# Kernel optimization log

Measured on AMD Instinct MI355X. Metric: run time of the kernel, lower is better.

## Reference

```python
import jax, jax.numpy as jnp
import numpy as np

ARITY = 4
DEPTH = 8          # leaves = ARITY**DEPTH = 65536; internal nodes = (4**8-1)//3 = 21845
IN_DIM = 64
MEM = 128
HID = 128


def setup_inputs() -> dict:
    key = jax.random.key(0)
    ks = jax.random.split(key, 20)
    n_leaves = ARITY ** DEPTH
    n_internal = (ARITY ** DEPTH - 1) // (ARITY - 1)
    s = 0.05
    inp = {
        "inputs": jax.random.normal(ks[0], (n_leaves, IN_DIM), jnp.float32),
        "ops": jax.random.randint(ks[1], (n_internal,), 0, 2, jnp.int32),
        # MLP (all bias-free); torch Linear weight layout [out, in]
        "W1": jax.random.normal(ks[2], (MEM, IN_DIM), jnp.float32) * s,
        "W2": jax.random.normal(ks[3], (3 * MEM, MEM), jnp.float32) * s,
        "W3": jax.random.normal(ks[4], (2 * MEM, 3 * MEM), jnp.float32) * s,
        "Wp": jax.random.normal(ks[5], (MEM, 2 * MEM), jnp.float32) * s,
        # ChildSumTreeRNN
        "Wand": jax.random.normal(ks[6], (MEM, MEM), jnp.float32) * s,
        "Wor": jax.random.normal(ks[7], (MEM, MEM), jnp.float32) * s,
        "Rw1": jax.random.normal(ks[8], (HID, MEM), jnp.float32) * s,
        "Rb1": jnp.zeros((HID,), jnp.float32),
        "Rw2": jax.random.normal(ks[9], (HID, HID), jnp.float32) * s,
        "Rb2": jnp.zeros((HID,), jnp.float32),
        "Rw3": jax.random.normal(ks[10], (HID, HID), jnp.float32) * s,
        "Rb3": jnp.zeros((HID,), jnp.float32),
        "Rwp": jax.random.normal(ks[11], (1, HID), jnp.float32) * s,
        "Rbp": jnp.zeros((1,), jnp.float32),
    }
    return inp


def reference(inputs, ops, W1, W2, W3, Wp, Wand, Wor,
              Rw1, Rb1, Rw2, Rb2, Rw3, Rb3, Rwp, Rbp):
    # MLP embedding of all leaves  [n_leaves, MEM]
    h = jnp.tanh(inputs @ W1.T)
    h = jnp.tanh(h @ W2.T)
    h = jnp.tanh(h @ W3.T)
    h = jnp.tanh(h @ Wp.T)

    # ChildSumTreeRNN, level by level (children before parents).
    # Complete arity-4 tree: level l has 4**l internal nodes; ops is
    # level-ordered from the root, so level l starts at (4**l - 1)//3.
    for l in range(DEPTH - 1, -1, -1):
        n = ARITY ** l
        start = (ARITY ** l - 1) // (ARITY - 1)
        ops_l = ops[start:start + n]                      # [n]
        ch = h.reshape(n, ARITY, MEM)                     # children states
        ha = jnp.tanh(jnp.einsum('ncm,om->nco', ch, Wand)).mean(axis=1)
        ho = jnp.tanh(jnp.einsum('ncm,om->nco', ch, Wor)).mean(axis=1)
        h = jnp.where((ops_l == 0)[:, None], ha, ho)      # [n, MEM]

    x = jax.nn.relu(h @ Rw1.T + Rb1)
    x = jax.nn.relu(x @ Rw2.T + Rb2)
    x = jax.nn.relu(x @ Rw3.T + Rb3)
    out = x @ Rwp.T + Rbp                                 # [1, 1]
    return out
```

## Files before the change

### kernel.cpp

```cpp
#include <hip/hip_runtime.h>
#include <hip/hip_bf16.h>
#include <stdint.h>

#define N_LEAVES 65536
#define MEM 128
#define HID 128

typedef float  f32x4 __attribute__((ext_vector_type(4)));
typedef short  s16x8 __attribute__((ext_vector_type(8)));
typedef unsigned short u16;
typedef u16    u16x8 __attribute__((ext_vector_type(8)));

__device__ __forceinline__ u16 f2bf(float x) {
    unsigned u = __builtin_bit_cast(unsigned, x);
    u += 0x7FFFu + ((u >> 16) & 1u);
    return (u16)(u >> 16);
}
__device__ __forceinline__ float bf2f(u16 b) {
    unsigned u = ((unsigned)b) << 16;
    return __builtin_bit_cast(float, u);
}
__device__ __forceinline__ float hif(float x) {
    return __builtin_bit_cast(float, __builtin_bit_cast(unsigned, x) & 0xffff0000u);
}
__device__ __forceinline__ unsigned packbf(float e0, float e1) {
    return __builtin_amdgcn_perm(__builtin_bit_cast(unsigned, e1),
                                 __builtin_bit_cast(unsigned, e0), 0x07060302u);
}
__device__ __forceinline__ float tanh_c(float x) {
    float E = __builtin_amdgcn_exp2f(x * 2.8853900817779268f);
    return 1.0f - 2.0f * __builtin_amdgcn_rcpf(E + 1.0f);
}
__device__ __forceinline__ float tanh_p(float x) {
    float x2 = x * x;
    float poly = x * (1.0f + x2 * (-0.33333334f + x2 * 0.13333334f));
    float E = __builtin_amdgcn_exp2f(x * 2.8853900817779268f);
    float ex = 1.0f - 2.0f * __builtin_amdgcn_rcpf(E + 1.0f);
    return (__builtin_fabsf(x) < 0.25f) ? poly : ex;
}

__device__ __forceinline__ f32x4 mfma_bf(s16x8 a, s16x8 b, f32x4 c) {
    return __builtin_amdgcn_mfma_f32_16x16x32_bf16(a, b, c, 0, 0, 0);
}

__global__ __launch_bounds__(256) void prep_all(
    const float* __restrict__ W1, const float* __restrict__ W2,
    const float* __restrict__ W3, const float* __restrict__ Wp,
    const float* __restrict__ Wand, const float* __restrict__ Wor,
    u16* __restrict__ w1tH, u16* __restrict__ w1tL,
    u16* __restrict__ w2tH, u16* __restrict__ w2tL,
    u16* __restrict__ w3tH, u16* __restrict__ w3tL,
    u16* __restrict__ wptH, u16* __restrict__ wptL,
    u16* __restrict__ waH,  u16* __restrict__ waL,
    u16* __restrict__ woH,  u16* __restrict__ woL)
{
    int g = blockIdx.x * 256 + threadIdx.x;
    const float* W; u16 *Th, *Tl; int K, N, base;
    if (g < 1024)       { W = W1;  Th = w1tH; Tl = w1tL; N = 128; K = 64;  base = 0; }
    else if (g < 7168)  { W = W2;  Th = w2tH; Tl = w2tL; N = 384; K = 128; base = 1024; }
    else if (g < 19456) { W = W3;  Th = w3tH; Tl = w3tL; N = 256; K = 384; base = 7168; }
    else if (g < 23552) { W = Wp;  Th = wptH; Tl = wptL; N = 128; K = 256; base = 19456; }
    else if (g < 25600) { W = Wand; Th = waH; Tl = waL;  N = 128; K = 128; base = 23552; }
    else if (g < 27648) { W = Wor;  Th = woH; Tl = woL;  N = 128; K = 128; base = 25600; }
    else return;
    int t = g - base;
    int kg8 = K >> 3;
    int n = t / kg8, kg = t - n * kg8;
    const float* src = &W[(size_t)n * K + kg * 8];
    size_t dst = ((size_t)kg * N + n) * 8;
    u16x8 hv, lv;
    #pragma unroll
    for (int j = 0; j < 8; ++j) {
        float v = src[j];
        u16 hb = f2bf(v);
        hv[j] = hb;
        lv[j] = f2bf(v - bf2f(hb));
    }
    *(u16x8*)&Th[dst] = hv;
    *(u16x8*)&Tl[dst] = lv;
}

__device__ __forceinline__ int act_g(int Wu, int row, int c4) {
    return row * (Wu >> 3) + (c4 ^ (row & 7));
}

template<int FJ, int KTN, int WINU, int WSTR, int D>
__device__ __forceinline__ void mlp_core(
    f32x4 (&acc)[FJ][2],
    const u16* inH, const u16* inL,
    const u16* __restrict__ BtH, const u16* __restrict__ BtL,
    int kt0, int rowBase, int featBase, int l)
{
    const int lr = l & 15, lc = l >> 4;
    s16x8 wh[D][FJ], wl[D][FJ];
    s16x8 ah[2][2], al[2][2];

    #pragma unroll
    for (int d = 0; d < D; ++d)
        #pragma unroll
        for (int fi = 0; fi < FJ; ++fi) {
            int o = (((kt0 + d) * 4 + lc) * WSTR + featBase + fi * 16 + lr) * 8;
            wh[d][fi] = *(const s16x8*)&BtH[o];
            wl[d][fi] = *(const s16x8*)&BtL[o];
        }
    #pragma unroll
    for (int rj = 0; rj < 2; ++rj) {
        int off = act_g(WINU, rowBase + rj * 16 + lr, lc) * 8;
        ah[0][rj] = *(const s16x8*)&inH[off];
        al[0][rj] = *(const s16x8*)&inL[off];
    }

    #pragma unroll
    for (int kt = 0; kt < KTN; ++kt) {
        const int ws_ = kt % D;
        const int as_ = kt & 1;
        if (kt + 1 < KTN) {
            #pragma unroll
            for (int rj = 0; rj < 2; ++rj) {
                int off = act_g(WINU, rowBase + rj * 16 + lr, (kt + 1) * 4 + lc) * 8;
                ah[as_ ^ 1][rj] = *(const s16x8*)&inH[off];
                al[as_ ^ 1][rj] = *(const s16x8*)&inL[off];
            }
        }
        #pragma unroll
        for (int fi = 0; fi < FJ; ++fi)
            #pragma unroll
            for (int rj = 0; rj < 2; ++rj) {
                f32x4 a = acc[fi][rj];
                a = mfma_bf(wh[ws_][fi], ah[as_][rj], a);
                a = mfma_bf(wh[ws_][fi], al[as_][rj], a);
                a = mfma_bf(wl[ws_][fi], ah[as_][rj], a);
                acc[fi][rj] = a;
            }
        if (kt + D < KTN) {
            #pragma unroll
            for (int fi = 0; fi < FJ; ++fi) {
                int o = (((kt0 + kt + D) * 4 + lc) * WSTR + featBase + fi * 16 + lr) * 8;
                wh[ws_][fi] = *(const s16x8*)&BtH[o];
                wl[ws_][fi] = *(const s16x8*)&BtL[o];
            }
        }
    }
}

template<int FJ, int WOUTU>
__device__ __forceinline__ void write_act(
    f32x4 (&acc)[FJ][2], u16* outH, u16* outL, int rowBase, int featBase, int l)
{
    const int lr = l & 15, lc = l >> 4;
    #pragma unroll
    for (int fi = 0; fi < FJ; ++fi)
        #pragma unroll
        for (int rj = 0; rj < 2; ++rj) {
            int m  = rowBase + rj * 16 + lr;
            int n0 = featBase + fi * 16 + lc * 4;
            f32x4 v = acc[fi][rj];
            float t0 = tanh_c(v[0]), t1 = tanh_c(v[1]);
            float t2 = tanh_c(v[2]), t3 = tanh_c(v[3]);
            uint2 hp, lp;
            hp.x = packbf(t0, t1);
            hp.y = packbf(t2, t3);
            lp.x = packbf(t0 - hif(t0), t1 - hif(t1));
            lp.y = packbf(t2 - hif(t2), t3 - hif(t3));
            int go = act_g(WOUTU, m, n0 >> 3) * 8 + (n0 & 7);
            *(uint2*)&outH[go] = hp;
            *(uint2*)&outL[go] = lp;
        }
}

template<int CJ, int FJ, bool TOGLOBAL>
__device__ __forceinline__ void tree_level(
    const u16* inH, const u16* inL,
    const u16* __restrict__ wAH, const u16* __restrict__ wAL,
    const u16* __restrict__ wOH, const u16* __restrict__ wOL,
    const int* __restrict__ opsL,
    u16* outH, u16* outL,
    int outRowBase, int nValid, int cfBase, int ffBase, int l)
{
    const int lr = l & 15, lc = l >> 4;
    f32x4 accA[CJ][FJ] = {};
    f32x4 accO[CJ][FJ] = {};

    #pragma unroll
    for (int kt = 0; kt < 4; ++kt) {
        s16x8 ah[CJ], al[CJ];
        #pragma unroll
        for (int c = 0; c < CJ; ++c) {
            int off = act_g(128, (cfBase + c) * 16 + lr, kt * 4 + lc) * 8;
            ah[c] = *(const s16x8*)&inH[off];
            al[c] = *(const s16x8*)&inL[off];
        }
        #pragma unroll
        for (int f = 0; f < FJ; ++f) {
            int wo = ((kt * 4 + lc) * 128 + ffBase + f * 16 + lr) * 8;
            s16x8 bah = *(const s16x8*)&wAH[wo];
            s16x8 bal = *(const s16x8*)&wAL[wo];
            s16x8 boh = *(const s16x8*)&wOH[wo];
            s16x8 bol = *(const s16x8*)&wOL[wo];
            #pragma unroll
            for (int c = 0; c < CJ; ++c) {
                f32x4 a = accA[c][f];
                a = mfma_bf(ah[c], bah, a);
                a = mfma_bf(ah[c], bal, a);
                a = mfma_bf(al[c], bah, a);
                accA[c][f] = a;
                f32x4 o = accO[c][f];
                o = mfma_bf(ah[c], boh, o);
                o = mfma_bf(ah[c], bol, o);
                o = mfma_bf(al[c], boh, o);
                accO[c][f] = o;
            }
        }
    }

    #pragma unroll
    for (int c = 0; c < CJ; ++c) {
        int p = (cfBase + c) * 4 + lc;
        if (p < nValid) {
            int op = opsL[p];
            #pragma unroll
            for (int f = 0; f < FJ; ++f) {
                f32x4 v = op ? accO[c][f] : accA[c][f];
                float t = 0.25f * (tanh_p(v[0]) + tanh_p(v[1]) + tanh_p(v[2]) + tanh_p(v[3]));
                unsigned bits = __builtin_bit_cast(unsigned, t);
                u16 hb = (u16)(bits >> 16);
                float lof = t - __builtin_bit_cast(float, bits & 0xffff0000u);
                u16 lb = (u16)(__builtin_bit_cast(unsigned, lof) >> 16);
                int feat = ffBase + f * 16 + lr;
                if constexpr (TOGLOBAL) {
                    int ga = (outRowBase + p) * 128 + feat;
                    outH[ga] = hb;
                    outL[ga] = lb;
                } else {
                    int go = act_g(128, outRowBase + p, feat >> 3) * 8 + (feat & 7);
                    outH[go] = hb;
                    outL[go] = lb;
                }
            }
        }
    }
}

__global__ __launch_bounds__(512, 4) void leaf_fused(
    const float* __restrict__ x,
    const u16* __restrict__ W1tH, const u16* __restrict__ W1tL,
    const u16* __restrict__ W2tH, const u16* __restrict__ W2tL,
    const u16* __restrict__ W3tH, const u16* __restrict__ W3tL,
    const u16* __restrict__ WptH, const u16* __restrict__ WptL,
    const u16* __restrict__ waH,  const u16* __restrict__ waL,
    const u16* __restrict__ woH,  const u16* __restrict__ woL,
    const int* __restrict__ ops,
    u16* __restrict__ l7H, u16* __restrict__ l7L)
{
    __shared__ u16 pool[32768];

    u16* h1H = pool;               u16* h1L = pool + 8192;
    u16* xH  = pool + 16384;       u16* xL  = pool + 20480;
    u16* h2H = pool + 16384;       u16* h2L = pool + 24576;
    u16* h3H = pool;               u16* h3L = pool + 16384;
    u16* h4H = pool;               u16* h4L = pool + 8192;

    const int tid = threadIdx.x;
    const int w = tid >> 6, l = tid & 63;
    const int rg = w >> 2;
    const int fg = w & 3;
    const int rowB = rg * 32;
    const int blk = blockIdx.x;
    const int rowBase = blk * 64;

    {
        int row = tid >> 3;
        int c0  = (tid & 7) * 8;
        const float* src = &x[(size_t)(rowBase + row) * 64 + c0];
        float4 v0 = *(const float4*)src;
        float4 v1 = *(const float4*)(src + 4);
        float xs[8] = {v0.x, v0.y, v0.z, v0.w, v1.x, v1.y, v1.z, v1.w};
        int go = act_g(64, row, c0 >> 3) * 8;
        uint4 hp, lp;
        hp.x = packbf(xs[0], xs[1]); hp.y = packbf(xs[2], xs[3]);
        hp.z = packbf(xs[4], xs[5]); hp.w = packbf(xs[6], xs[7]);
        lp.x = packbf(xs[0] - hif(xs[0]), xs[1] - hif(xs[1]));
        lp.y = packbf(xs[2] - hif(xs[2]), xs[3] - hif(xs[3]));
        lp.z = packbf(xs[4] - hif(xs[4]), xs[5] - hif(xs[5]));
        lp.w = packbf(xs[6] - hif(xs[6]), xs[7] - hif(xs[7]));
        *(uint4*)&xH[go] = hp;
        *(uint4*)&xL[go] = lp;
    }
    __syncthreads();

    {
        f32x4 acc1[2][2] = {};
        mlp_core<2, 2, 64, 128, 2>(acc1, xH, xL, W1tH, W1tL, 0, rowB, fg * 32, l);
        write_act<2, 128>(acc1, h1H, h1L, rowB, fg * 32, l);
    }
    __syncthreads();

    f32x4 acc3[4][2] = {};
    #pragma unroll
    for (int p = 0; p < 3; ++p) {
        if (p) __syncthreads();
        {
            f32x4 acc2[2][2] = {};
            mlp_core<2, 4, 128, 384, 2>(acc2, h1H, h1L, W2tH, W2tL, 0,
                                        rowB, p * 128 + fg * 32, l);
            write_act<2, 128>(acc2, h2H, h2L, rowB, fg * 32, l);
        }
        __syncthreads();
        mlp_core<4, 4, 128, 256, 1>(acc3, h2H, h2L, W3tH, W3tL, p * 4,
                                    rowB, fg * 64, l);
    }
    __syncthreads();
    write_act<4, 256>(acc3, h3H, h3L, rowB, fg * 64, l);
    __syncthreads();

    {
        f32x4 acc4[2][2] = {};
        mlp_core<2, 8, 256, 128, 2>(acc4, h3H, h3L, WptH, WptL, 0, rowB, fg * 32, l);
        __syncthreads();
        write_act<2, 128>(acc4, h4H, h4L, rowB, fg * 32, l);
    }
    __syncthreads();

    tree_level<1, 4, true>(h4H, h4L, waH, waL, woH, woL,
                           ops + 5461 + blk * 16, l7H, l7L,
                           blk * 16, 16, (w >> 1), (w & 1) * 64, l);
}

__global__ __launch_bounds__(512, 4) void tree3(
    const u16* __restrict__ inH, const u16* __restrict__ inL,
    const u16* __restrict__ wAH, const u16* __restrict__ wAL,
    const u16* __restrict__ wOH, const u16* __restrict__ wOL,
    const int* __restrict__ ops0, const int* __restrict__ ops1,
    const int* __restrict__ ops2,
    u16* __restrict__ outH, u16* __restrict__ outL)
{
    __shared__ u16 L0H[16384], L0L[16384];
    __shared__ u16 L1H[4096],  L1L[4096];

    const int tid = threadIdx.x;
    const int w = tid >> 6, l = tid & 63;
    const int blk = blockIdx.x;

    #pragma unroll
    for (int it = 0; it < 4; ++it) {
        int g = tid + it * 512;
        int row = g >> 4, c4 = g & 15;
        size_t src = (size_t)(blk * 128 + row) * 128 + c4 * 8;
        int dst = act_g(128, row, c4) * 8;
        *(u16x8*)&L0H[dst] = *(const u16x8*)&inH[src];
        *(u16x8*)&L0L[dst] = *(const u16x8*)&inL[src];
    }
    __syncthreads();

    tree_level<2, 4, false>(L0H, L0L, wAH, wAL, wOH, wOL, ops0 + blk * 32,
                            L1H, L1L, 0, 32, (w & 3) * 2, (w >> 2) * 64, l);
    __syncthreads();
    tree_level<1, 2, false>(L1H, L1L, wAH, wAL, wOH, wOL, ops1 + blk * 8,
                            L0H, L0L, 0, 8, (w >> 2), (w & 3) * 32, l);
    __syncthreads();
    tree_level<1, 1, true>(L0H, L0L, wAH, wAL, wOH, wOL, ops2 + blk * 2,
                           outH, outL, blk * 2, 2, 0, w * 16, l);
}

__global__ __launch_bounds__(128) void tail_final(
    const u16* __restrict__ l1H, const u16* __restrict__ l1L,
    const int* __restrict__ ops,
    const float* __restrict__ Wand, const float* __restrict__ Wor,
    const float* __restrict__ Rw1, const float* __restrict__ Rb1,
    const float* __restrict__ Rw2, const float* __restrict__ Rb2,
    const float* __restrict__ Rw3, const float* __restrict__ Rb3,
    const float* __restrict__ Rwp, const float* __restrict__ Rbp,
    float* __restrict__ out)
{
    __shared__ float h[512];
    __shared__ float F[512];
    const int o = threadIdx.x;

    for (int i = o; i < 512; i += 128) h[i] = bf2f(l1H[i]) + bf2f(l1L[i]);
    __syncthreads();

    {
        const float* Wsel = (ops[0] == 0) ? Wand : Wor;
        const float4* wr = (const float4*)&Wsel[o * 128];
        const float4* h0 = (const float4*)&h[0];
        const float4* h1 = (const float4*)&h[128];
        const float4* h2 = (const float4*)&h[256];
        const float4* h3 = (const float4*)&h[384];
        float s0 = 0, s1 = 0, s2 = 0, s3 = 0;
        for (int m = 0; m < 32; ++m) {
            float4 wv = wr[m];
            float4 a0 = h0[m], a1 = h1[m], a2 = h2[m], a3 = h3[m];
            s0 += wv.x*a0.x + wv.y*a0.y + wv.z*a0.z + wv.w*a0.w;
            s1 += wv.x*a1.x + wv.y*a1.y + wv.z*a1.z + wv.w*a1.w;
            s2 += wv.x*a2.x + wv.y*a2.y + wv.z*a2.z + wv.w*a2.w;
            s3 += wv.x*a3.x + wv.y*a3.y + wv.z*a3.z + wv.w*a3.w;
        }
        F[o] = 0.25f * (tanh_p(s0) + tanh_p(s1) + tanh_p(s2) + tanh_p(s3));
    }
    __syncthreads();
    {
        const float4* wr = (const float4*)&Rw1[o * 128];
        const float4* xr = (const float4*)&F[0];
        float s = 0;
        for (int m = 0; m < 32; ++m) {
            float4 wv = wr[m], xv = xr[m];
            s += wv.x*xv.x + wv.y*xv.y + wv.z*xv.z + wv.w*xv.w;
        }
        __syncthreads();
        F[128 + o] = fmaxf(s + Rb1[o], 0.f);
    }
    __syncthreads();
    {
        const float4* wr = (const float4*)&Rw2[o * 128];
        const float4* xr = (const float4*)&F[128];
        float s = 0;
        for (int m = 0; m < 32; ++m) {
            float4 wv = wr[m], xv = xr[m];
            s += wv.x*xv.x + wv.y*xv.y + wv.z*xv.z + wv.w*xv.w;
        }
        __syncthreads();
        F[256 + o] = fmaxf(s + Rb2[o], 0.f);
    }
    __syncthreads();
    {
        const float4* wr = (const float4*)&Rw3[o * 128];
        const float4* xr = (const float4*)&F[256];
        float s = 0;
        for (int m = 0; m < 32; ++m) {
            float4 wv = wr[m], xv = xr[m];
            s += wv.x*xv.x + wv.y*xv.y + wv.z*xv.z + wv.w*xv.w;
        }
        __syncthreads();
        F[384 + o] = fmaxf(s + Rb3[o], 0.f) * Rwp[o];
    }
    __syncthreads();
    if (o == 0) {
        float t = 0.f;
        for (int i = 0; i < 128; ++i) t += F[384 + i];
        out[0] = t + Rbp[0];
    }
}

extern "C" void kernel_launch(void* const* d_in, const int* in_sizes, int n_in,
                              void* d_out, int out_size, void* d_ws, size_t ws_size,
                              hipStream_t stream)
{
    const float* inputs = (const float*)d_in[0];
    const int*   ops    = (const int*)d_in[1];
    const float* W1     = (const float*)d_in[2];
    const float* W2     = (const float*)d_in[3];
    const float* W3     = (const float*)d_in[4];
    const float* Wp     = (const float*)d_in[5];
    const float* Wand   = (const float*)d_in[6];
    const float* Wor    = (const float*)d_in[7];
    const float* Rw1    = (const float*)d_in[8];
    const float* Rb1    = (const float*)d_in[9];
    const float* Rw2    = (const float*)d_in[10];
    const float* Rb2    = (const float*)d_in[11];
    const float* Rw3    = (const float*)d_in[12];
    const float* Rb3    = (const float*)d_in[13];
    const float* Rwp    = (const float*)d_in[14];
    const float* Rbp    = (const float*)d_in[15];
    float* out = (float*)d_out;
    u16* ws = (u16*)d_ws;

    size_t off = 0;
    u16* w1tH = ws + off; off += 8192;   u16* w1tL = ws + off; off += 8192;
    u16* w2tH = ws + off; off += 49152;  u16* w2tL = ws + off; off += 49152;
    u16* w3tH = ws + off; off += 98304;  u16* w3tL = ws + off; off += 98304;
    u16* wptH = ws + off; off += 32768;  u16* wptL = ws + off; off += 32768;
    u16* waH  = ws + off; off += 16384;  u16* waL  = ws + off; off += 16384;
    u16* woH  = ws + off; off += 16384;  u16* woL  = ws + off; off += 16384;
    u16* l7H  = ws + off; off += (size_t)16384 * 128;
    u16* l7L  = ws + off; off += (size_t)16384 * 128;
    u16* l4H  = ws + off; off += 256 * 128;
    u16* l4L  = ws + off; off += 256 * 128;
    u16* l1H  = ws + off; off += 512;
    u16* l1L  = ws + off; off += 512;

    prep_all<<<108, 256, 0, stream>>>(W1, W2, W3, Wp, Wand, Wor,
        w1tH, w1tL, w2tH, w2tL, w3tH, w3tL, wptH, wptL, waH, waL, woH, woL);

    leaf_fused<<<N_LEAVES / 64, 512, 0, stream>>>(
        inputs, w1tH, w1tL, w2tH, w2tL, w3tH, w3tL, wptH, wptL,
        waH, waL, woH, woL, ops, l7H, l7L);

    tree3<<<128, 512, 0, stream>>>(l7H, l7L, waH, waL, woH, woL,
        ops + 1365, ops + 341, ops + 85, l4H, l4L);

    tree3<<<2, 512, 0, stream>>>(l4H, l4L, waH, waL, woH, woL,
        ops + 21, ops + 5, ops + 1, l1H, l1L);

    tail_final<<<1, 128, 0, stream>>>(l1H, l1L, ops, Wand, Wor,
        Rw1, Rb1, Rw2, Rb2, Rw3, Rb3, Rwp, Rbp, out);
}
```

Before: 138.1 us.

## Shrink leaf kernel to 32-row blocks with chunked h3 staging to cut LDS

The fused leaf kernel now processes 32 rows per block with 256 threads (4 waves, each owning a feature slice) instead of 64 rows with 512 threads. The h3 activation is no longer written in full to shared memory; it is staged in two 128-wide chunks into a reused buffer, and the Wp projection accumulates over the chunks. Shared memory per block halves and launch bounds target more resident blocks, aiming for better occupancy and latency hiding. In exchange, weights are reloaded per block across twice as many blocks, and the extra barriers and the tree-level mapping change add per-block overhead.

```diff
diff --git a/kernel.cpp b/kernel.cpp
--- a/kernel.cpp
+++ b/kernel.cpp
@@ -89,7 +89,7 @@
     f32x4 (&acc)[FJ][2],
     const u16* inH, const u16* inL,
     const u16* __restrict__ BtH, const u16* __restrict__ BtL,
-    int kt0, int rowBase, int featBase, int l)
+    int kt0, int featBase, int l)
 {
     const int lr = l & 15, lc = l >> 4;
     s16x8 wh[D][FJ], wl[D][FJ];
@@ -105,7 +105,7 @@
         }
     #pragma unroll
     for (int rj = 0; rj < 2; ++rj) {
-        int off = act_g(WINU, rowBase + rj * 16 + lr, lc) * 8;
+        int off = act_g(WINU, rj * 16 + lr, lc) * 8;
         ah[0][rj] = *(const s16x8*)&inH[off];
         al[0][rj] = *(const s16x8*)&inL[off];
     }
@@ -117,7 +117,7 @@
         if (kt + 1 < KTN) {
             #pragma unroll
             for (int rj = 0; rj < 2; ++rj) {
-                int off = act_g(WINU, rowBase + rj * 16 + lr, (kt + 1) * 4 + lc) * 8;
+                int off = act_g(WINU, rj * 16 + lr, (kt + 1) * 4 + lc) * 8;
                 ah[as_ ^ 1][rj] = *(const s16x8*)&inH[off];
                 al[as_ ^ 1][rj] = *(const s16x8*)&inL[off];
             }
@@ -145,14 +145,14 @@
 
 template<int FJ, int WOUTU>
 __device__ __forceinline__ void write_act(
-    f32x4 (&acc)[FJ][2], u16* outH, u16* outL, int rowBase, int featBase, int l)
+    f32x4 (&acc)[FJ][2], u16* outH, u16* outL, int featBase, int l)
 {
     const int lr = l & 15, lc = l >> 4;
     #pragma unroll
     for (int fi = 0; fi < FJ; ++fi)
         #pragma unroll
         for (int rj = 0; rj < 2; ++rj) {
-            int m  = rowBase + rj * 16 + lr;
+            int m  = rj * 16 + lr;
             int n0 = featBase + fi * 16 + lc * 4;
             f32x4 v = acc[fi][rj];
             float t0 = tanh_c(v[0]), t1 = tanh_c(v[1]);
@@ -241,7 +241,7 @@
     }
 }
 
-__global__ __launch_bounds__(512, 4) void leaf_fused(
+__global__ __launch_bounds__(256, 6) void leaf_fused(
     const float* __restrict__ x,
     const u16* __restrict__ W1tH, const u16* __restrict__ W1tL,
     const u16* __restrict__ W2tH, const u16* __restrict__ W2tL,
@@ -252,21 +252,18 @@
     const int* __restrict__ ops,
     u16* __restrict__ l7H, u16* __restrict__ l7L)
 {
-    __shared__ u16 pool[32768];
-
-    u16* h1H = pool;               u16* h1L = pool + 8192;
-    u16* xH  = pool + 16384;       u16* xL  = pool + 20480;
-    u16* h2H = pool + 16384;       u16* h2L = pool + 24576;
-    u16* h3H = pool;               u16* h3L = pool + 16384;
-    u16* h4H = pool;               u16* h4L = pool + 8192;
+    __shared__ u16 pool[16384];
+
+    u16* ckH = pool;               u16* ckL = pool + 4096;
+    u16* xH  = pool;               u16* xL  = pool + 2048;
+    u16* h1H = pool + 8192;        u16* h1L = pool + 12288;
+    u16* h4H = pool + 8192;        u16* h4L = pool + 12288;
 
     const int tid = threadIdx.x;
     const int w = tid >> 6, l = tid & 63;
-    const int rg = w >> 2;
-    const int fg = w & 3;
-    const int rowB = rg * 32;
+    const int fg = w;
     const int blk = blockIdx.x;
-    const int rowBase = blk * 64;
+    const int rowBase = blk * 32;
 
     {
         int row = tid >> 3;
@@ -290,8 +287,8 @@
 
     {
         f32x4 acc1[2][2] = {};
-        mlp_core<2, 2, 64, 128, 2>(acc1, xH, xL, W1tH, W1tL, 0, rowB, fg * 32, l);
-        write_act<2, 128>(acc1, h1H, h1L, rowB, fg * 32, l);
+        mlp_core<2, 2, 64, 128, 2>(acc1, xH, xL, W1tH, W1tL, 0, fg * 32, l);
+        write_act<2, 128>(acc1, h1H, h1L, fg * 32, l);
     }
     __syncthreads();
 
@@ -302,28 +299,32 @@
         {
             f32x4 acc2[2][2] = {};
             mlp_core<2, 4, 128, 384, 2>(acc2, h1H, h1L, W2tH, W2tL, 0,
-                                        rowB, p * 128 + fg * 32, l);
-            write_act<2, 128>(acc2, h2H, h2L, rowB, fg * 32, l);
-        }
-        __syncthreads();
-        mlp_core<4, 4, 128, 256, 1>(acc3, h2H, h2L, W3tH, W3tL, p * 4,
-                                    rowB, fg * 64, l);
-    }
-    __syncthreads();
-    write_act<4, 256>(acc3, h3H, h3L, rowB, fg * 64, l);
-    __syncthreads();
-
-    {
-        f32x4 acc4[2][2] = {};
-        mlp_core<2, 8, 256, 128, 2>(acc4, h3H, h3L, WptH, WptL, 0, rowB, fg * 32, l);
-        __syncthreads();
-        write_act<2, 128>(acc4, h4H, h4L, rowB, fg * 32, l);
-    }
-    __syncthreads();
-
-    tree_level<1, 4, true>(h4H, h4L, waH, waL, woH, woL,
-                           ops + 5461 + blk * 16, l7H, l7L,
-                           blk * 16, 16, (w >> 1), (w & 1) * 64, l);
+                                        p * 128 + fg * 32, l);
+            write_act<2, 128>(acc2, ckH, ckL, fg * 32, l);
+        }
+        __syncthreads();
+        mlp_core<4, 4, 128, 256, 1>(acc3, ckH, ckL, W3tH, W3tL, p * 4,
+                                    fg * 64, l);
+    }
+
+    f32x4 acc4[2][2] = {};
+    #pragma unroll
+    for (int c = 0; c < 2; ++c) {
+        __syncthreads();
+        if ((w >> 1) == c) {
+            write_act<4, 128>(acc3, ckH, ckL, (fg & 1) * 64, l);
+        }
+        __syncthreads();
+        mlp_core<2, 4, 128, 128, 2>(acc4, ckH, ckL, WptH, WptL, c * 4,
+                                    fg * 32, l);
+    }
+    __syncthreads();
+    write_act<2, 128>(acc4, h4H, h4L, fg * 32, l);
+    __syncthreads();
+
+    tree_level<2, 2, true>(h4H, h4L, waH, waL, woH, woL,
+                           ops + 5461 + blk * 8, l7H, l7L,
+                           blk * 8, 8, 0, fg * 32, l);
 }
 
 __global__ __launch_bounds__(512, 4) void tree3(
@@ -481,7 +482,7 @@
     prep_all<<<108, 256, 0, stream>>>(W1, W2, W3, Wp, Wand, Wor,
         w1tH, w1tL, w2tH, w2tL, w3tH, w3tL, wptH, wptL, waH, waL, woH, woL);
 
-    leaf_fused<<<N_LEAVES / 64, 512, 0, stream>>>(
+    leaf_fused<<<N_LEAVES / 32, 256, 0, stream>>>(
         inputs, w1tH, w1tL, w2tH, w2tL, w3tH, w3tL, wptH, wptL,
         waH, waL, woH, woL, ops, l7H, l7L);
 
```

New measurement: 142.0 us. 2.8% more time.
